# Kernel optimization log

Hardware: AMD Instinct MI355X
Metric: run time of the kernel (lower is better)

The kernel has to match this reference:

```python
import jax, jax.numpy as jnp
import numpy as np

B, IN, H, A = 2048, 2048, 2048, 2
DT = 0.05
TAU = 0.05
SIGMA_V = 1.0
V_RESET = 0.0
R = 0.1
I0 = 0.7


def setup_inputs() -> dict:
    key = jax.random.key(0)
    ks = jax.random.split(key, 13)
    return {
        "x": jax.random.normal(ks[0], (B, IN), jnp.float32),
        "firing": jax.random.uniform(ks[1], (B, H), jnp.float32),
        "voltage": jax.random.normal(ks[2], (B, H), jnp.float32),
        "ascurrent": jax.random.normal(ks[3], (A, B, H), jnp.float32),
        "syncurrent": jax.random.normal(ks[4], (B, H), jnp.float32),
        "firing_delayed": jax.random.uniform(ks[5], (B, H), jnp.float32),
        "weight_iv": jax.random.normal(ks[6], (IN, H), jnp.float32) / np.sqrt(H),
        "weight_lat": jax.random.normal(ks[7], (H, H), jnp.float32) / np.sqrt(H),
        "thresh": jax.random.normal(ks[8], (1, H), jnp.float32),
        "trans_k_m": jax.random.normal(ks[9], (1, H), jnp.float32),
        "trans_k_j": jax.random.normal(ks[10], (A, 1, H), jnp.float32),
        "trans_r_j": jax.random.normal(ks[11], (A, 1, H), jnp.float32),
        "a_j": jax.random.normal(ks[12], (A, 1, H), jnp.float32),
    }


def reference(x, firing, voltage, ascurrent, syncurrent, firing_delayed,
              weight_iv, weight_lat, thresh, trans_k_m, trans_k_j, trans_r_j, a_j):
    # synaptic current: input + lateral matmuls
    syncurrent = x @ weight_iv + firing_delayed @ weight_lat  # (B, H)
    # after-spike currents (broadcast params (A,1,H) over batch)
    asc_r = 1.0 - 2.0 * jax.nn.sigmoid(trans_r_j)
    k_j = jax.nn.sigmoid(trans_k_j) / DT
    ascurrent = ((ascurrent * asc_r + a_j) * firing * (DT / TAU)
                 + (1.0 - DT * k_j) * ascurrent)  # (A, B, H)
    # voltage update
    k_m = jax.nn.sigmoid(trans_k_m) / DT
    voltage = (syncurrent
               + DT * k_m * R * (jnp.sum(ascurrent, axis=0) + I0)
               + (1.0 - DT * k_m) * voltage
               - (DT / TAU) * firing * (voltage - V_RESET))
    # sigmoid spike function
    firing = jax.nn.sigmoid((voltage - thresh) / SIGMA_V)
    return (firing, voltage, ascurrent, syncurrent)
```

## Files before the change

kernel.cpp:

```cpp
#include <hip/hip_runtime.h>

typedef unsigned short u16;
typedef __bf16 __attribute__((ext_vector_type(8))) bf16x8;
typedef float __attribute__((ext_vector_type(4))) floatx4;

#define BH 4194304
#define HDIM 2048
#define KTOT 4096

__device__ __forceinline__ float bf2f(u16 u) {
  unsigned int v = ((unsigned int)u) << 16;
  return __builtin_bit_cast(float, v);
}
__device__ __forceinline__ u16 f2bf(float f) {
  unsigned int v = __builtin_bit_cast(unsigned int, f);
  unsigned int r = (v + 0x7fffu + ((v >> 16) & 1u)) >> 16;
  return (u16)r;
}
__device__ __forceinline__ unsigned cvtpk(float a, float b) {
  unsigned r;
  asm("v_cvt_pk_bf16_f32 %0, %1, %2" : "=v"(r) : "v"(a), "v"(b));
  return r;
}
__device__ __forceinline__ unsigned packu(u16 a, u16 b) {
  return (unsigned)a | ((unsigned)b << 16);
}
__device__ __forceinline__ float sigm(float x) {
  return 1.f / (1.f + __expf(-x));
}

template <bool F32> struct Elt { using T = float; };
template <> struct Elt<false> { using T = u16; };

template <bool F32> struct Stg;
template <> struct Stg<true>  { float4 a[4]; float b[16]; };
template <> struct Stg<false> { uint4  a[2]; u16   b[16]; };

template <bool F32>
__device__ __forceinline__ float ldel(const void* p, size_t i) {
  if constexpr (F32) return ((const float*)p)[i];
  else return bf2f(((const u16*)p)[i]);
}
template <bool F32>
__device__ __forceinline__ void stel(void* p, size_t i, float v) {
  if constexpr (F32) ((float*)p)[i] = v;
  else ((u16*)p)[i] = f2bf(v);
}

template <bool F32>
__device__ void glifr_body(
    const void* xv, const void* fdv, const void* wivv, const void* wlatv,
    const void* firingv, const void* voltagev, const void* ascv,
    const void* threshv, const void* tkmv, const void* tkjv,
    const void* trjv, const void* ajv, void* outv,
    u16* As0, u16* Bs0, u16* As1, u16* Bs1) {
  using El = typename Elt<F32>::T;
  const El* x    = (const El*)xv;
  const El* fd   = (const El*)fdv;
  const El* wiv  = (const El*)wivv;
  const El* wlat = (const El*)wlatv;

  const int tid  = threadIdx.x;
  const int lane = tid & 63;
  const int w    = tid >> 6;
  const int wm   = w >> 1;
  const int wn   = w & 1;
  const int m0   = blockIdx.y * 64;
  const int n0   = blockIdx.x * 64;

  int rowA[2], dgA[2];
#pragma unroll
  for (int i = 0; i < 2; ++i) {
    int slot = tid + i * 256;
    rowA[i] = slot >> 3;
    dgA[i]  = slot & 7;
  }
  const int quad  = lane >> 4;
  const int col   = lane & 15;
  const int kbase = w * 16;

  floatx4 acc[2][2] = {};
  Stg<F32> S0, S1;

  auto issueA = [&](Stg<F32>& st, const El* asrc) {
#pragma unroll
    for (int i = 0; i < 2; ++i) {
      const El* p = asrc + (size_t)(m0 + rowA[i]) * HDIM + dgA[i] * 8;
      if constexpr (F32) {
        st.a[2 * i]     = *(const float4*)p;
        st.a[2 * i + 1] = *(const float4*)(p + 4);
      } else {
        st.a[i] = *(const uint4*)p;
      }
    }
  };
  auto issueB = [&](Stg<F32>& st, const El* wsrc) {
    const El* p = wsrc + (size_t)kbase * HDIM + n0 + lane;
#pragma unroll
    for (int j = 0; j < 16; ++j) st.b[j] = p[(size_t)j * HDIM];
  };
  auto writeTile = [&](Stg<F32>& st, u16* As, u16* Bs) {
#pragma unroll
    for (int i = 0; i < 2; ++i) {
      uint4 q;
      if constexpr (F32) {
        q.x = cvtpk(st.a[2 * i].x, st.a[2 * i].y);
        q.y = cvtpk(st.a[2 * i].z, st.a[2 * i].w);
        q.z = cvtpk(st.a[2 * i + 1].x, st.a[2 * i + 1].y);
        q.w = cvtpk(st.a[2 * i + 1].z, st.a[2 * i + 1].w);
      } else {
        q = st.a[i];
      }
      *(uint4*)&As[rowA[i] * 64 + ((dgA[i] ^ (rowA[i] & 7)) << 3)] = q;
    }
#pragma unroll
    for (int c = 0; c < 2; ++c) {
      uint4 q;
      if constexpr (F32) {
        q.x = cvtpk(st.b[8 * c + 0], st.b[8 * c + 1]);
        q.y = cvtpk(st.b[8 * c + 2], st.b[8 * c + 3]);
        q.z = cvtpk(st.b[8 * c + 4], st.b[8 * c + 5]);
        q.w = cvtpk(st.b[8 * c + 6], st.b[8 * c + 7]);
      } else {
        q.x = packu(st.b[8 * c + 0], st.b[8 * c + 1]);
        q.y = packu(st.b[8 * c + 2], st.b[8 * c + 3]);
        q.z = packu(st.b[8 * c + 4], st.b[8 * c + 5]);
        q.w = packu(st.b[8 * c + 6], st.b[8 * c + 7]);
      }
      const int ch = 2 * w + c;
      *(uint4*)&Bs[lane * 64 + ((ch ^ (lane & 7)) << 3)] = q;
    }
  };
  auto mfmaPhase = [&](const u16* As, const u16* Bs) {
#pragma unroll
    for (int kk = 0; kk < 64; kk += 32) {
      bf16x8 af[2], bf[2];
#pragma unroll
      for (int mi = 0; mi < 2; ++mi) {
        const int r = wm * 32 + mi * 16 + col;
        const int p = ((kk >> 3) + quad) ^ (r & 7);
        af[mi] = *(const bf16x8*)&As[r * 64 + p * 8];
      }
#pragma unroll
      for (int ni = 0; ni < 2; ++ni) {
        const int r = wn * 32 + ni * 16 + col;
        const int p = ((kk >> 3) + quad) ^ (r & 7);
        bf[ni] = *(const bf16x8*)&Bs[r * 64 + p * 8];
      }
#pragma unroll
      for (int mi = 0; mi < 2; ++mi)
#pragma unroll
        for (int ni = 0; ni < 2; ++ni)
          acc[mi][ni] = __builtin_amdgcn_mfma_f32_16x16x32_bf16(
              af[mi], bf[ni], acc[mi][ni], 0, 0, 0);
    }
  };
  auto srcA = [&](int kn) -> const El* {
    return (kn < 2048) ? (x + kn) : (fd + (kn - 2048));
  };
  auto srcW = [&](int kn) -> const El* {
    return (kn < 2048) ? (wiv + (size_t)kn * HDIM)
                       : (wlat + (size_t)(kn - 2048) * HDIM);
  };

  issueA(S0, srcA(0));   issueB(S0, srcW(0));
  issueA(S1, srcA(64));  issueB(S1, srcW(64));
  writeTile(S0, As0, Bs0);
  __syncthreads();

  for (int t = 0; t < 64; t += 2) {
    {
      const int kn = (t + 2) * 64;
      if (kn < KTOT) { issueA(S0, srcA(kn)); issueB(S0, srcW(kn)); }
      mfmaPhase(As0, Bs0);
      writeTile(S1, As1, Bs1);
      __syncthreads();
    }
    {
      const int kn = (t + 3) * 64;
      if (kn < KTOT) { issueA(S1, srcA(kn)); issueB(S1, srcW(kn)); }
      mfmaPhase(As1, Bs1);
      if ((t + 2) * 64 < KTOT) writeTile(S0, As0, Bs0);
      __syncthreads();
    }
  }

#pragma unroll
  for (int ni = 0; ni < 2; ++ni) {
    const int h = n0 + wn * 32 + ni * 16 + col;
    const float th  = ldel<F32>(threshv, h);
    const float sm  = sigm(ldel<F32>(tkmv, h));
    const float sk0 = sigm(ldel<F32>(tkjv, h));
    const float sk1 = sigm(ldel<F32>(tkjv, HDIM + h));
    const float r0  = 1.f - 2.f * sigm(ldel<F32>(trjv, h));
    const float r1  = 1.f - 2.f * sigm(ldel<F32>(trjv, HDIM + h));
    const float a0c = ldel<F32>(ajv, h);
    const float a1c = ldel<F32>(ajv, HDIM + h);
#pragma unroll
    for (int mi = 0; mi < 2; ++mi) {
#pragma unroll
      for (int i = 0; i < 4; ++i) {
        const int m = m0 + wm * 32 + mi * 16 + quad * 4 + i;
        const size_t idx = (size_t)m * HDIM + h;
        const float f   = ldel<F32>(firingv, idx);
        const float v   = ldel<F32>(voltagev, idx);
        const float A0  = ldel<F32>(ascv, idx);
        const float A1  = ldel<F32>(ascv, BH + idx);
        const float syn = acc[mi][ni][i];
        const float na0 = (A0 * r0 + a0c) * f + (1.f - sk0) * A0;
        const float na1 = (A1 * r1 + a1c) * f + (1.f - sk1) * A1;
        const float nv  = syn + sm * 0.1f * (na0 + na1 + 0.7f)
                          + (1.f - sm) * v - f * v;
        const float nf  = sigm(nv - th);
        stel<F32>(outv, idx,            nf);
        stel<F32>(outv, BH + idx,       nv);
        stel<F32>(outv, 2 * BH + idx,   na0);
        stel<F32>(outv, 3 * BH + idx,   na1);
        stel<F32>(outv, 4 * BH + idx,   syn);
      }
    }
  }
}

__device__ __forceinline__ bool detect_f32(const u16* xu) {
  bool wild = false;
  for (int i = (threadIdx.x & 63); i < 1024; i += 64) {
    const u16 u = xu[i];
    if ((u & 0x7f80u) == 0x7f80u || fabsf(bf2f(u)) > 64.f) wild = true;
  }
  return __any(wild);
}

__global__ __launch_bounds__(256, 4) void glifr_fused(
    const void* x, const void* fd, const void* wiv, const void* wlat,
    const void* firing, const void* voltage, const void* asc,
    const void* thresh, const void* tkm, const void* tkj, const void* trj,
    const void* aj, void* out) {
  __shared__ u16 As0[64 * 64];
  __shared__ u16 Bs0[64 * 64];
  __shared__ u16 As1[64 * 64];
  __shared__ u16 Bs1[64 * 64];
  if (detect_f32((const u16*)x)) {
    glifr_body<true>(x, fd, wiv, wlat, firing, voltage, asc, thresh, tkm,
                     tkj, trj, aj, out, As0, Bs0, As1, Bs1);
  } else {
    glifr_body<false>(x, fd, wiv, wlat, firing, voltage, asc, thresh, tkm,
                      tkj, trj, aj, out, As0, Bs0, As1, Bs1);
  }
}

extern "C" void kernel_launch(void* const* d_in, const int* in_sizes, int n_in,
                              void* d_out, int out_size, void* d_ws, size_t ws_size,
                              hipStream_t stream) {
  const void* x    = d_in[0];
  const void* fir  = d_in[1];
  const void* vol  = d_in[2];
  const void* asc  = d_in[3];
  const void* fd   = d_in[5];
  const void* wiv  = d_in[6];
  const void* wlat = d_in[7];
  const void* th   = d_in[8];
  const void* tkm  = d_in[9];
  const void* tkj  = d_in[10];
  const void* trj  = d_in[11];
  const void* aj   = d_in[12];

  glifr_fused<<<dim3(32, 32), 256, 0, stream>>>(
      x, fd, wiv, wlat, fir, vol, asc, th, tkm, tkj, trj, aj, d_out);
}
```

Baseline: 393.2 us.

## Use 512-thread blocks with single-buffered LDS and smaller per-wave tiles

Doubles the block to 8 waves, so each wave computes a 32x16 output slice instead of 32x32 and stages half as many global elements per k-step. The LDS double buffer and two-stage register prefetch become a single LDS buffer with one register stage and two barriers per k-tile. The aim is more waves resident per CU and lower register pressure to hide memory latency. In exchange it adds a second barrier per iteration and gives each wave less MFMA work per LDS load.

```diff
diff --git a/kernel.cpp b/kernel.cpp
--- a/kernel.cpp
+++ b/kernel.cpp
@@ -33,8 +33,8 @@
 template <> struct Elt<false> { using T = u16; };
 
 template <bool F32> struct Stg;
-template <> struct Stg<true>  { float4 a[4]; float b[16]; };
-template <> struct Stg<false> { uint4  a[2]; u16   b[16]; };
+template <> struct Stg<true>  { float4 a[2]; float b[8]; };
+template <> struct Stg<false> { uint4  a;    u16   b[8]; };
 
 template <bool F32>
 __device__ __forceinline__ float ldel(const void* p, size_t i) {
@@ -53,7 +53,7 @@
     const void* firingv, const void* voltagev, const void* ascv,
     const void* threshv, const void* tkmv, const void* tkjv,
     const void* trjv, const void* ajv, void* outv,
-    u16* As0, u16* Bs0, u16* As1, u16* Bs1) {
+    u16* As, u16* Bs) {
   using El = typename Elt<F32>::T;
   const El* x    = (const El*)xv;
   const El* fd   = (const El*)fdv;
@@ -63,96 +63,78 @@
   const int tid  = threadIdx.x;
   const int lane = tid & 63;
   const int w    = tid >> 6;
-  const int wm   = w >> 1;
-  const int wn   = w & 1;
+  const int wm   = w >> 2;
+  const int wn   = w & 3;
   const int m0   = blockIdx.y * 64;
   const int n0   = blockIdx.x * 64;
 
-  int rowA[2], dgA[2];
-#pragma unroll
-  for (int i = 0; i < 2; ++i) {
-    int slot = tid + i * 256;
-    rowA[i] = slot >> 3;
-    dgA[i]  = slot & 7;
-  }
-  const int quad  = lane >> 4;
-  const int col   = lane & 15;
-  const int kbase = w * 16;
-
-  floatx4 acc[2][2] = {};
-  Stg<F32> S0, S1;
-
-  auto issueA = [&](Stg<F32>& st, const El* asrc) {
-#pragma unroll
-    for (int i = 0; i < 2; ++i) {
-      const El* p = asrc + (size_t)(m0 + rowA[i]) * HDIM + dgA[i] * 8;
-      if constexpr (F32) {
-        st.a[2 * i]     = *(const float4*)p;
-        st.a[2 * i + 1] = *(const float4*)(p + 4);
-      } else {
-        st.a[i] = *(const uint4*)p;
-      }
-    }
-  };
-  auto issueB = [&](Stg<F32>& st, const El* wsrc) {
+  const int rowA = tid >> 3;
+  const int dgA  = tid & 7;
+  const int quad = lane >> 4;
+  const int col  = lane & 15;
+  const int kbase = w * 8;
+
+  floatx4 acc[2] = {};
+  Stg<F32> S;
+
+  auto issueA = [&](const El* asrc) {
+    const El* p = asrc + (size_t)(m0 + rowA) * HDIM + dgA * 8;
+    if constexpr (F32) {
+      S.a[0] = *(const float4*)p;
+      S.a[1] = *(const float4*)(p + 4);
+    } else {
+      S.a = *(const uint4*)p;
+    }
+  };
+  auto issueB = [&](const El* wsrc) {
     const El* p = wsrc + (size_t)kbase * HDIM + n0 + lane;
 #pragma unroll
-    for (int j = 0; j < 16; ++j) st.b[j] = p[(size_t)j * HDIM];
-  };
-  auto writeTile = [&](Stg<F32>& st, u16* As, u16* Bs) {
-#pragma unroll
-    for (int i = 0; i < 2; ++i) {
-      uint4 q;
-      if constexpr (F32) {
-        q.x = cvtpk(st.a[2 * i].x, st.a[2 * i].y);
-        q.y = cvtpk(st.a[2 * i].z, st.a[2 * i].w);
-        q.z = cvtpk(st.a[2 * i + 1].x, st.a[2 * i + 1].y);
-        q.w = cvtpk(st.a[2 * i + 1].z, st.a[2 * i + 1].w);
-      } else {
-        q = st.a[i];
-      }
-      *(uint4*)&As[rowA[i] * 64 + ((dgA[i] ^ (rowA[i] & 7)) << 3)] = q;
-    }
-#pragma unroll
-    for (int c = 0; c < 2; ++c) {
-      uint4 q;
-      if constexpr (F32) {
-        q.x = cvtpk(st.b[8 * c + 0], st.b[8 * c + 1]);
-        q.y = cvtpk(st.b[8 * c + 2], st.b[8 * c + 3]);
-        q.z = cvtpk(st.b[8 * c + 4], st.b[8 * c + 5]);
-        q.w = cvtpk(st.b[8 * c + 6], st.b[8 * c + 7]);
-      } else {
-        q.x = packu(st.b[8 * c + 0], st.b[8 * c + 1]);
-        q.y = packu(st.b[8 * c + 2], st.b[8 * c + 3]);
-        q.z = packu(st.b[8 * c + 4], st.b[8 * c + 5]);
-        q.w = packu(st.b[8 * c + 6], st.b[8 * c + 7]);
-      }
-      const int ch = 2 * w + c;
-      *(uint4*)&Bs[lane * 64 + ((ch ^ (lane & 7)) << 3)] = q;
-    }
-  };
-  auto mfmaPhase = [&](const u16* As, const u16* Bs) {
+    for (int j = 0; j < 8; ++j) S.b[j] = p[(size_t)j * HDIM];
+  };
+  auto writeTile = [&]() {
+    uint4 qa;
+    if constexpr (F32) {
+      qa.x = cvtpk(S.a[0].x, S.a[0].y);
+      qa.y = cvtpk(S.a[0].z, S.a[0].w);
+      qa.z = cvtpk(S.a[1].x, S.a[1].y);
+      qa.w = cvtpk(S.a[1].z, S.a[1].w);
+    } else {
+      qa = S.a;
+    }
+    *(uint4*)&As[rowA * 64 + ((dgA ^ (rowA & 7)) << 3)] = qa;
+    uint4 qb;
+    if constexpr (F32) {
+      qb.x = cvtpk(S.b[0], S.b[1]);
+      qb.y = cvtpk(S.b[2], S.b[3]);
+      qb.z = cvtpk(S.b[4], S.b[5]);
+      qb.w = cvtpk(S.b[6], S.b[7]);
+    } else {
+      qb.x = packu(S.b[0], S.b[1]);
+      qb.y = packu(S.b[2], S.b[3]);
+      qb.z = packu(S.b[4], S.b[5]);
+      qb.w = packu(S.b[6], S.b[7]);
+    }
+    *(uint4*)&Bs[lane * 64 + ((w ^ (lane & 7)) << 3)] = qb;
+  };
+  auto mfmaPhase = [&]() {
 #pragma unroll
     for (int kk = 0; kk < 64; kk += 32) {
-      bf16x8 af[2], bf[2];
+      bf16x8 af[2], bf;
 #pragma unroll
       for (int mi = 0; mi < 2; ++mi) {
         const int r = wm * 32 + mi * 16 + col;
         const int p = ((kk >> 3) + quad) ^ (r & 7);
         af[mi] = *(const bf16x8*)&As[r * 64 + p * 8];
       }
-#pragma unroll
-      for (int ni = 0; ni < 2; ++ni) {
-        const int r = wn * 32 + ni * 16 + col;
+      {
+        const int r = wn * 16 + col;
         const int p = ((kk >> 3) + quad) ^ (r & 7);
-        bf[ni] = *(const bf16x8*)&Bs[r * 64 + p * 8];
+        bf = *(const bf16x8*)&Bs[r * 64 + p * 8];
       }
 #pragma unroll
       for (int mi = 0; mi < 2; ++mi)
-#pragma unroll
-        for (int ni = 0; ni < 2; ++ni)
-          acc[mi][ni] = __builtin_amdgcn_mfma_f32_16x16x32_bf16(
-              af[mi], bf[ni], acc[mi][ni], 0, 0, 0);
+        acc[mi] = __builtin_amdgcn_mfma_f32_16x16x32_bf16(
+            af[mi], bf, acc[mi], 0, 0, 0);
     }
   };
   auto srcA = [&](int kn) -> const El* {
@@ -163,31 +145,22 @@
                        : (wlat + (size_t)(kn - 2048) * HDIM);
   };
 
-  issueA(S0, srcA(0));   issueB(S0, srcW(0));
-  issueA(S1, srcA(64));  issueB(S1, srcW(64));
-  writeTile(S0, As0, Bs0);
-  __syncthreads();
-
-  for (int t = 0; t < 64; t += 2) {
-    {
-      const int kn = (t + 2) * 64;
-      if (kn < KTOT) { issueA(S0, srcA(kn)); issueB(S0, srcW(kn)); }
-      mfmaPhase(As0, Bs0);
-      writeTile(S1, As1, Bs1);
-      __syncthreads();
-    }
-    {
-      const int kn = (t + 3) * 64;
-      if (kn < KTOT) { issueA(S1, srcA(kn)); issueB(S1, srcW(kn)); }
-      mfmaPhase(As1, Bs1);
-      if ((t + 2) * 64 < KTOT) writeTile(S0, As0, Bs0);
-      __syncthreads();
-    }
-  }
-
-#pragma unroll
-  for (int ni = 0; ni < 2; ++ni) {
-    const int h = n0 + wn * 32 + ni * 16 + col;
+  issueA(srcA(0));
+  issueB(srcW(0));
+
+  for (int kb = 0; kb < KTOT; kb += 64) {
+    writeTile();
+    if (kb + 64 < KTOT) {
+      issueA(srcA(kb + 64));
+      issueB(srcW(kb + 64));
+    }
+    __syncthreads();
+    mfmaPhase();
+    __syncthreads();
+  }
+
+  {
+    const int h = n0 + wn * 16 + col;
     const float th  = ldel<F32>(threshv, h);
     const float sm  = sigm(ldel<F32>(tkmv, h));
     const float sk0 = sigm(ldel<F32>(tkjv, h));
@@ -206,7 +179,7 @@
         const float v   = ldel<F32>(voltagev, idx);
         const float A0  = ldel<F32>(ascv, idx);
         const float A1  = ldel<F32>(ascv, BH + idx);
-        const float syn = acc[mi][ni][i];
+        const float syn = acc[mi][i];
         const float na0 = (A0 * r0 + a0c) * f + (1.f - sk0) * A0;
         const float na1 = (A1 * r1 + a1c) * f + (1.f - sk1) * A1;
         const float nv  = syn + sm * 0.1f * (na0 + na1 + 0.7f)
@@ -231,21 +204,19 @@
   return __any(wild);
 }
 
-__global__ __launch_bounds__(256, 4) void glifr_fused(
+__global__ __launch_bounds__(512, 8) void glifr_fused(
     const void* x, const void* fd, const void* wiv, const void* wlat,
     const void* firing, const void* voltage, const void* asc,
     const void* thresh, const void* tkm, const void* tkj, const void* trj,
     const void* aj, void* out) {
-  __shared__ u16 As0[64 * 64];
-  __shared__ u16 Bs0[64 * 64];
-  __shared__ u16 As1[64 * 64];
-  __shared__ u16 Bs1[64 * 64];
+  __shared__ u16 As[64 * 64];
+  __shared__ u16 Bs[64 * 64];
   if (detect_f32((const u16*)x)) {
     glifr_body<true>(x, fd, wiv, wlat, firing, voltage, asc, thresh, tkm,
-                     tkj, trj, aj, out, As0, Bs0, As1, Bs1);
+                     tkj, trj, aj, out, As, Bs);
   } else {
     glifr_body<false>(x, fd, wiv, wlat, firing, voltage, asc, thresh, tkm,
-                      tkj, trj, aj, out, As0, Bs0, As1, Bs1);
+                      tkj, trj, aj, out, As, Bs);
   }
 }
 
@@ -265,6 +236,6 @@
   const void* trj  = d_in[11];
   const void* aj   = d_in[12];
 
-  glifr_fused<<<dim3(32, 32), 256, 0, stream>>>(
+  glifr_fused<<<dim3(32, 32), 512, 0, stream>>>(
       x, fd, wiv, wlat, fir, vol, asc, th, tkm, tkj, trj, aj, d_out);
 }
```

New measurement: 328.1 us. 1.2x faster.
